# Optimization experiments

Measured on AMD Instinct MI355X. Metric: run time of the kernel, lower is better.

## Reference

```python
import jax, jax.numpy as jnp
import numpy as np

DIM = 1024
HID = 4 * DIM
N_EXPERTS = 8
TOP_K = 2


def setup_inputs() -> dict:
    key = jax.random.key(0)
    ks = jax.random.split(key, 8)
    s = lambda fan_in: 1.0 / np.sqrt(fan_in)
    x = jax.random.normal(ks[0], (2, 2048, DIM), dtype=jnp.float32)
    Wr = jax.random.uniform(ks[1], (DIM, N_EXPERTS), jnp.float32, -s(DIM), s(DIM))
    br = jnp.zeros((N_EXPERTS,), jnp.float32)
    W1 = jax.random.uniform(ks[2], (N_EXPERTS, DIM, HID), jnp.float32, -s(DIM), s(DIM))
    b1 = jnp.zeros((N_EXPERTS, HID), jnp.float32)
    W2 = jax.random.uniform(ks[3], (N_EXPERTS, HID, DIM), jnp.float32, -s(HID), s(HID))
    b2 = jnp.zeros((N_EXPERTS, DIM), jnp.float32)
    return {"x": x, "Wr": Wr, "br": br, "W1": W1, "b1": b1, "W2": W2, "b2": b2}


def reference(x, Wr, br, W1, b1, W2, b2):
    B, S, D = x.shape
    xf = x.reshape(-1, D)                      # [T, D]
    T = xf.shape[0]
    logits = xf @ Wr + br                      # [T, E]
    topw, sel = jax.lax.top_k(logits, TOP_K)   # [T, k]
    topw = jax.nn.softmax(topw, axis=-1)       # softmax over selected experts only
    # dense per-token, per-expert weight (0 for unselected experts)
    w_full = jnp.zeros((T, N_EXPERTS), xf.dtype).at[jnp.arange(T)[:, None], sel].add(topw)
    # run every expert densely (reference baseline), weighted combine
    h = jax.nn.gelu(jnp.einsum('td,edh->teh', xf, W1) + b1, approximate=False)  # [T,E,H]
    y = jnp.einsum('teh,ehd->ted', h, W2) + b2                                   # [T,E,D]
    out = jnp.einsum('ted,te->td', y, w_full)
    return out.reshape(B, S, D)
```

## Files before the change

### kernel.cpp

```cpp
#include <hip/hip_runtime.h>
#include <math.h>

#define DIM 1024
#define HID 4096
#define NE 8
#define NTOK 4096

typedef short s16x8 __attribute__((ext_vector_type(8)));
typedef float f32x4 __attribute__((ext_vector_type(4)));

__device__ __forceinline__ unsigned short f2bf(float f) {
  unsigned int u = __float_as_uint(f);
  u = u + 0x7fffu + ((u >> 16) & 1u);
  return (unsigned short)(u >> 16);
}

__device__ __forceinline__ void gll16(const void* g, void* l) {
  __builtin_amdgcn_global_load_lds(
      (const __attribute__((address_space(1))) unsigned int*)g,
      (__attribute__((address_space(3))) unsigned int*)l, 16, 0, 0);
}

__global__ __launch_bounds__(256) void zero_k(float4* out4, int* ctrl) {
  int i = blockIdx.x * 256 + threadIdx.x;
  out4[i] = make_float4(0.f, 0.f, 0.f, 0.f);
  if (i < 32) ctrl[i] = 0;
}

__global__ __launch_bounds__(256) void router_k(const float* __restrict__ x,
    const float* __restrict__ Wr, const float* __restrict__ br,
    short* __restrict__ xbf, int* __restrict__ ctrl,
    int* __restrict__ sel, float* __restrict__ selw) {
  __shared__ float lred[4 * NE];
  int t = blockIdx.x, tid = threadIdx.x;
  const float* xr = x + (size_t)t * DIM;
  float p[NE];
#pragma unroll
  for (int e = 0; e < NE; ++e) p[e] = 0.f;
#pragma unroll
  for (int it = 0; it < DIM / 256; ++it) {
    int d = it * 256 + tid;
    float xv = xr[d];
    xbf[(size_t)t * DIM + d] = (short)f2bf(xv);
#pragma unroll
    for (int e = 0; e < NE; ++e) p[e] += xv * Wr[d * NE + e];
  }
#pragma unroll
  for (int e = 0; e < NE; ++e) {
    float v = p[e];
#pragma unroll
    for (int off = 32; off > 0; off >>= 1) v += __shfl_down(v, off);
    if ((tid & 63) == 0) lred[(tid >> 6) * NE + e] = v;
  }
  __syncthreads();
  if (tid == 0) {
    float lg[NE];
#pragma unroll
    for (int e = 0; e < NE; ++e)
      lg[e] = lred[e] + lred[NE + e] + lred[2 * NE + e] + lred[3 * NE + e] + br[e];
    int b0 = 0; float v0 = lg[0];
    for (int e = 1; e < NE; ++e) if (lg[e] > v0) { v0 = lg[e]; b0 = e; }
    int b1i = -1; float v1 = -3.4e38f;
    for (int e = 0; e < NE; ++e) if (e != b0 && lg[e] > v1) { v1 = lg[e]; b1i = e; }
    float e1 = expf(v1 - v0);
    float inv = 1.f / (1.f + e1);
    sel[t * 2] = b0; sel[t * 2 + 1] = b1i;
    selw[t * 2] = inv; selw[t * 2 + 1] = e1 * inv;
    atomicAdd(&ctrl[b0], 1); atomicAdd(&ctrl[b1i], 1);
  }
}

__global__ void scan_k(int* ctrl) {
  if (threadIdx.x == 0) {
    int o = 0;
#pragma unroll
    for (int e = 0; e < NE; ++e) { ctrl[8 + e] = o; o += ctrl[e]; }
    ctrl[16] = o;
  }
}

__global__ __launch_bounds__(256) void build_k(const int* __restrict__ sel,
    const float* __restrict__ selw, int* ctrl,
    int* __restrict__ slot_tok, float* __restrict__ slot_w) {
  int t = blockIdx.x * 256 + threadIdx.x;
  if (t >= NTOK) return;
#pragma unroll
  for (int k = 0; k < 2; ++k) {
    int e = sel[t * 2 + k];
    int pos = atomicAdd(&ctrl[20 + e], 1);
    int s = ctrl[8 + e] + pos;
    slot_tok[s] = t;
    slot_w[s] = selw[t * 2 + k];
  }
}

__global__ __launch_bounds__(256) void tcvt_k(const float* __restrict__ src,
    short* __restrict__ dst, int K, int N) {
  __shared__ __attribute__((aligned(16))) short t[64][72];
  int e = blockIdx.z;
  int n0 = blockIdx.x * 64, k0 = blockIdx.y * 64;
  const float* s = src + (size_t)e * K * N;
  short* d = dst + (size_t)e * N * K;
  int tid = threadIdx.x;
#pragma unroll
  for (int i = 0; i < 4; ++i) {
    int c = tid + i * 256;
    int row = c >> 4, c4 = c & 15;
    float4 v = *(const float4*)&s[(size_t)(k0 + row) * N + n0 + c4 * 4];
    t[c4 * 4 + 0][row] = (short)f2bf(v.x);
    t[c4 * 4 + 1][row] = (short)f2bf(v.y);
    t[c4 * 4 + 2][row] = (short)f2bf(v.z);
    t[c4 * 4 + 3][row] = (short)f2bf(v.w);
  }
  __syncthreads();
#pragma unroll
  for (int i = 0; i < 2; ++i) {
    int c = tid + i * 256;
    int n = c >> 3, k8 = c & 7;
    *(s16x8*)&d[(size_t)(n0 + n) * K + k0 + k8 * 8] = *(const s16x8*)&t[n][k8 * 8];
  }
}

__global__ __launch_bounds__(256) void gemm1n_k(const short* __restrict__ xbf,
    const short* __restrict__ w1t, const float* __restrict__ b1,
    const int* __restrict__ ctrl, const int* __restrict__ slot_tok,
    short* __restrict__ h) {
  int e = blockIdx.z, my = blockIdx.y, bx = blockIdx.x;
  int cnt = ctrl[e];
  if (my * 128 >= cnt) return;
  int slot0 = ctrl[8 + e];
  int tid = threadIdx.x, lane = tid & 63;
  int wv = tid >> 6, wm = wv >> 1, wn = wv & 1;
  __shared__ __attribute__((aligned(16))) short ldsA[2][128 * 32];
  __shared__ __attribute__((aligned(16))) short ldsB[2][128 * 32];

  const short* ga[2]; const short* gb[2]; int lo[2];
#pragma unroll
  for (int i = 0; i < 2; ++i) {
    int c = tid + i * 256;
    int row = c >> 2;
    int cs = (c & 3) ^ (row & 3);
    int srow = min(my * 128 + row, cnt - 1);
    ga[i] = xbf + (size_t)slot_tok[slot0 + srow] * DIM + cs * 8;
    gb[i] = w1t + ((size_t)e * HID + bx * 128 + row) * DIM + cs * 8;
    lo[i] = c * 8;
  }
  int koff = ((lane >> 4) ^ (lane & 3)) * 8;

  f32x4 acc[4][4];
#pragma unroll
  for (int i = 0; i < 4; ++i)
#pragma unroll
    for (int j = 0; j < 4; ++j) acc[i][j] = (f32x4){0.f, 0.f, 0.f, 0.f};

#pragma unroll
  for (int i = 0; i < 2; ++i) { gll16(ga[i], &ldsA[0][lo[i]]); gll16(gb[i], &ldsB[0][lo[i]]); }
  __syncthreads();

  const int NT = DIM / 32;
  for (int t = 0; t < NT; ++t) {
    int buf = t & 1;
    if (t + 1 < NT) {
      int nb = buf ^ 1;
#pragma unroll
      for (int i = 0; i < 2; ++i) {
        gll16(ga[i] + (t + 1) * 32, &ldsA[nb][lo[i]]);
        gll16(gb[i] + (t + 1) * 32, &ldsB[nb][lo[i]]);
      }
    }
    s16x8 aF[4], bF[4];
#pragma unroll
    for (int i = 0; i < 4; ++i)
      aF[i] = *(const s16x8*)&ldsA[buf][(wm * 64 + i * 16 + (lane & 15)) * 32 + koff];
#pragma unroll
    for (int j = 0; j < 4; ++j)
      bF[j] = *(const s16x8*)&ldsB[buf][(wn * 64 + j * 16 + (lane & 15)) * 32 + koff];
#pragma unroll
    for (int i = 0; i < 4; ++i)
#pragma unroll
      for (int j = 0; j < 4; ++j)
        acc[i][j] = __builtin_amdgcn_mfma_f32_16x16x32_bf16(aF[i], bF[j], acc[i][j], 0, 0, 0);
    __syncthreads();
  }
#pragma unroll
  for (int i = 0; i < 4; ++i) {
#pragma unroll
    for (int r = 0; r < 4; ++r) {
      int row_l = wm * 64 + i * 16 + (lane >> 4) * 4 + r;
      int grow = my * 128 + row_l;
      if (grow < cnt) {
#pragma unroll
        for (int j = 0; j < 4; ++j) {
          int col = bx * 128 + wn * 64 + j * 16 + (lane & 15);
          float z = acc[i][j][r] + b1[e * HID + col];
          float g = 0.5f * z * (1.f + erff(z * 0.70710678118f));
          h[(size_t)(slot0 + grow) * HID + col] = (short)f2bf(g);
        }
      }
    }
  }
}

__global__ __launch_bounds__(256) void gemm2n_k(const short* __restrict__ h,
    const short* __restrict__ w2t, const float* __restrict__ b2,
    const int* __restrict__ ctrl, const int* __restrict__ slot_tok,
    const float* __restrict__ slot_w, float* __restrict__ out) {
  int e = blockIdx.z, my = blockIdx.y;
  int nx = blockIdx.x & 7, kc = blockIdx.x >> 3;
  int cnt = ctrl[e];
  if (my * 128 >= cnt) return;
  int slot0 = ctrl[8 + e];
  int tid = threadIdx.x, lane = tid & 63;
  int wv = tid >> 6, wm = wv >> 1, wn = wv & 1;
  __shared__ __attribute__((aligned(16))) short ldsA[2][128 * 32];
  __shared__ __attribute__((aligned(16))) short ldsB[2][128 * 32];
  __shared__ int stok[128];
  __shared__ float swt[128];
  if (tid < 128) {
    int srow = min(my * 128 + tid, cnt - 1);
    stok[tid] = slot_tok[slot0 + srow];
    swt[tid] = slot_w[slot0 + srow];
  }
  int k0 = kc * (HID / 4);
  const short* ga[2]; const short* gb[2]; int lo[2];
#pragma unroll
  for (int i = 0; i < 2; ++i) {
    int c = tid + i * 256;
    int row = c >> 2;
    int cs = (c & 3) ^ (row & 3);
    int srow = min(my * 128 + row, cnt - 1);
    ga[i] = h + (size_t)(slot0 + srow) * HID + k0 + cs * 8;
    gb[i] = w2t + ((size_t)e * DIM + nx * 128 + row) * HID + k0 + cs * 8;
    lo[i] = c * 8;
  }
  int koff = ((lane >> 4) ^ (lane & 3)) * 8;

  f32x4 acc[4][4];
#pragma unroll
  for (int i = 0; i < 4; ++i)
#pragma unroll
    for (int j = 0; j < 4; ++j) acc[i][j] = (f32x4){0.f, 0.f, 0.f, 0.f};

#pragma unroll
  for (int i = 0; i < 2; ++i) { gll16(ga[i], &ldsA[0][lo[i]]); gll16(gb[i], &ldsB[0][lo[i]]); }
  __syncthreads();

  const int NT = (HID / 4) / 32;
  for (int t = 0; t < NT; ++t) {
    int buf = t & 1;
    if (t + 1 < NT) {
      int nb = buf ^ 1;
#pragma unroll
      for (int i = 0; i < 2; ++i) {
        gll16(ga[i] + (t + 1) * 32, &ldsA[nb][lo[i]]);
        gll16(gb[i] + (t + 1) * 32, &ldsB[nb][lo[i]]);
      }
    }
    s16x8 aF[4], bF[4];
#pragma unroll
    for (int i = 0; i < 4; ++i)
      aF[i] = *(const s16x8*)&ldsA[buf][(wm * 64 + i * 16 + (lane & 15)) * 32 + koff];
#pragma unroll
    for (int j = 0; j < 4; ++j)
      bF[j] = *(const s16x8*)&ldsB[buf][(wn * 64 + j * 16 + (lane & 15)) * 32 + koff];
#pragma unroll
    for (int i = 0; i < 4; ++i)
#pragma unroll
      for (int j = 0; j < 4; ++j)
        acc[i][j] = __builtin_amdgcn_mfma_f32_16x16x32_bf16(aF[i], bF[j], acc[i][j], 0, 0, 0);
    __syncthreads();
  }
#pragma unroll
  for (int i = 0; i < 4; ++i) {
#pragma unroll
    for (int r = 0; r < 4; ++r) {
      int row_l = wm * 64 + i * 16 + (lane >> 4) * 4 + r;
      int grow = my * 128 + row_l;
      if (grow < cnt) {
        int tok = stok[row_l];
        float wrow = swt[row_l];
#pragma unroll
        for (int j = 0; j < 4; ++j) {
          int col = nx * 128 + wn * 64 + j * 16 + (lane & 15);
          float y = acc[i][j][r];
          if (kc == 0) y += b2[e * DIM + col];
          unsafeAtomicAdd(&out[(size_t)tok * DIM + col], wrow * y);
        }
      }
    }
  }
}

__global__ __launch_bounds__(256) void gemm1_k(const short* __restrict__ xbf,
    const float* __restrict__ W1, const float* __restrict__ b1,
    const int* __restrict__ ctrl, const int* __restrict__ slot_tok,
    short* __restrict__ h) {
  int e = blockIdx.z, my = blockIdx.y, bx = blockIdx.x;
  int cnt = ctrl[e];
  if (my * 128 >= cnt) return;
  int slot0 = ctrl[8 + e];
  int tid = threadIdx.x, lane = tid & 63;
  int wv = tid >> 6, wm = wv >> 1, wn = wv & 1;
  __shared__ __attribute__((aligned(16))) short ldsA[128 * 32];
  __shared__ __attribute__((aligned(16))) short ldsB[128 * 40];
  const short* ap[2]; short* la[2];
#pragma unroll
  for (int i = 0; i < 2; ++i) {
    int c = tid + i * 256;
    int row = c >> 2;
    int srow = min(my * 128 + row, cnt - 1);
    int tok = slot_tok[slot0 + srow];
    ap[i] = xbf + (size_t)tok * DIM + (c & 3) * 8;
    la[i] = &ldsA[c * 8];
  }
  int n0 = (tid & 63) * 2;
  int kg = tid >> 6;
  const float* bp = W1 + ((size_t)e * DIM + kg * 8) * HID + bx * 128 + n0;
  short* lb0 = &ldsB[(n0) * 40 + kg * 8];
  short* lb1 = &ldsB[(n0 + 1) * 40 + kg * 8];
  f32x4 acc[4][4];
#pragma unroll
  for (int i = 0; i < 4; ++i)
#pragma unroll
    for (int j = 0; j < 4; ++j) acc[i][j] = (f32x4){0.f, 0.f, 0.f, 0.f};
#pragma unroll 2
  for (int kt = 0; kt < DIM / 32; ++kt) {
    float2 fv[8];
#pragma unroll
    for (int kk = 0; kk < 8; ++kk) fv[kk] = *(const float2*)&bp[(size_t)kk * HID];
    __syncthreads();
    gll16(ap[0], la[0]); gll16(ap[1], la[1]);
    s16x8 v0, v1;
#pragma unroll
    for (int kk = 0; kk < 8; ++kk) { v0[kk] = (short)f2bf(fv[kk].x); v1[kk] = (short)f2bf(fv[kk].y); }
    *(s16x8*)lb0 = v0; *(s16x8*)lb1 = v1;
    asm volatile("s_waitcnt vmcnt(0)" ::: "memory");
    __syncthreads();
    s16x8 aF[4], bF[4];
#pragma unroll
    for (int i = 0; i < 4; ++i)
      aF[i] = *(const s16x8*)&ldsA[(wm * 64 + i * 16 + (lane & 15)) * 32 + (lane >> 4) * 8];
#pragma unroll
    for (int j = 0; j < 4; ++j)
      bF[j] = *(const s16x8*)&ldsB[(wn * 64 + j * 16 + (lane & 15)) * 40 + (lane >> 4) * 8];
#pragma unroll
    for (int i = 0; i < 4; ++i)
#pragma unroll
      for (int j = 0; j < 4; ++j)
        acc[i][j] = __builtin_amdgcn_mfma_f32_16x16x32_bf16(aF[i], bF[j], acc[i][j], 0, 0, 0);
    ap[0] += 32; ap[1] += 32; bp += (size_t)32 * HID;
  }
#pragma unroll
  for (int i = 0; i < 4; ++i)
#pragma unroll
    for (int r = 0; r < 4; ++r) {
      int row_l = wm * 64 + i * 16 + (lane >> 4) * 4 + r;
      int grow = my * 128 + row_l;
      if (grow < cnt)
#pragma unroll
        for (int j = 0; j < 4; ++j) {
          int col = bx * 128 + wn * 64 + j * 16 + (lane & 15);
          float z = acc[i][j][r] + b1[e * HID + col];
          float g = 0.5f * z * (1.f + erff(z * 0.70710678118f));
          h[(size_t)(slot0 + grow) * HID + col] = (short)f2bf(g);
        }
    }
}

__global__ __launch_bounds__(256) void gemm2_k(const short* __restrict__ h,
    const float* __restrict__ W2, const float* __restrict__ b2,
    const int* __restrict__ ctrl, const int* __restrict__ slot_tok,
    const float* __restrict__ slot_w, float* __restrict__ out) {
  int e = blockIdx.z, my = blockIdx.y, bx = blockIdx.x;
  int cnt = ctrl[e];
  if (my * 128 >= cnt) return;
  int slot0 = ctrl[8 + e];
  int tid = threadIdx.x, lane = tid & 63;
  int wv = tid >> 6, wm = wv >> 1, wn = wv & 1;
  __shared__ __attribute__((aligned(16))) short ldsA[128 * 32];
  __shared__ __attribute__((aligned(16))) short ldsB[128 * 40];
  __shared__ int stok[128];
  __shared__ float swt[128];
  if (tid < 128) {
    int srow = min(my * 128 + tid, cnt - 1);
    stok[tid] = slot_tok[slot0 + srow];
    swt[tid] = slot_w[slot0 + srow];
  }
  const short* ap[2]; short* la[2];
#pragma unroll
  for (int i = 0; i < 2; ++i) {
    int c = tid + i * 256;
    int row = c >> 2;
    int srow = min(my * 128 + row, cnt - 1);
    ap[i] = h + (size_t)(slot0 + srow) * HID + (c & 3) * 8;
    la[i] = &ldsA[c * 8];
  }
  int n0 = (tid & 63) * 2;
  int kg = tid >> 6;
  const float* bp = W2 + ((size_t)e * HID + kg * 8) * DIM + bx * 128 + n0;
  short* lb0 = &ldsB[(n0) * 40 + kg * 8];
  short* lb1 = &ldsB[(n0 + 1) * 40 + kg * 8];
  f32x4 acc[4][4];
#pragma unroll
  for (int i = 0; i < 4; ++i)
#pragma unroll
    for (int j = 0; j < 4; ++j) acc[i][j] = (f32x4){0.f, 0.f, 0.f, 0.f};
#pragma unroll 2
  for (int kt = 0; kt < HID / 32; ++kt) {
    float2 fv[8];
#pragma unroll
    for (int kk = 0; kk < 8; ++kk) fv[kk] = *(const float2*)&bp[(size_t)kk * DIM];
    __syncthreads();
    gll16(ap[0], la[0]); gll16(ap[1], la[1]);
    s16x8 v0, v1;
#pragma unroll
    for (int kk = 0; kk < 8; ++kk) { v0[kk] = (short)f2bf(fv[kk].x); v1[kk] = (short)f2bf(fv[kk].y); }
    *(s16x8*)lb0 = v0; *(s16x8*)lb1 = v1;
    asm volatile("s_waitcnt vmcnt(0)" ::: "memory");
    __syncthreads();
    s16x8 aF[4], bF[4];
#pragma unroll
    for (int i = 0; i < 4; ++i)
      aF[i] = *(const s16x8*)&ldsA[(wm * 64 + i * 16 + (lane & 15)) * 32 + (lane >> 4) * 8];
#pragma unroll
    for (int j = 0; j < 4; ++j)
      bF[j] = *(const s16x8*)&ldsB[(wn * 64 + j * 16 + (lane & 15)) * 40 + (lane >> 4) * 8];
#pragma unroll
    for (int i = 0; i < 4; ++i)
#pragma unroll
      for (int j = 0; j < 4; ++j)
        acc[i][j] = __builtin_amdgcn_mfma_f32_16x16x32_bf16(aF[i], bF[j], acc[i][j], 0, 0, 0);
    ap[0] += 32; ap[1] += 32; bp += (size_t)32 * DIM;
  }
#pragma unroll
  for (int i = 0; i < 4; ++i)
#pragma unroll
    for (int r = 0; r < 4; ++r) {
      int row_l = wm * 64 + i * 16 + (lane >> 4) * 4 + r;
      int grow = my * 128 + row_l;
      if (grow < cnt) {
        int tok = stok[row_l];
        float wrow = swt[row_l];
#pragma unroll
        for (int j = 0; j < 4; ++j) {
          int col = bx * 128 + wn * 64 + j * 16 + (lane & 15);
          float y = acc[i][j][r] + b2[e * DIM + col];
          unsafeAtomicAdd(&out[(size_t)tok * DIM + col], wrow * y);
        }
      }
    }
}

extern "C" void kernel_launch(void* const* d_in, const int* in_sizes, int n_in,
                              void* d_out, int out_size, void* d_ws, size_t ws_size,
                              hipStream_t stream) {
  const float* x  = (const float*)d_in[0];
  const float* Wr = (const float*)d_in[1];
  const float* br = (const float*)d_in[2];
  const float* W1 = (const float*)d_in[3];
  const float* b1 = (const float*)d_in[4];
  const float* W2 = (const float*)d_in[5];
  const float* b2 = (const float*)d_in[6];
  float* out = (float*)d_out;

  char* ws = (char*)d_ws;
  const size_t MiB = 1024 * 1024;
  int*   ctrl     = (int*)(ws);
  int*   sel      = (int*)(ws + 1024);
  float* selw     = (float*)(ws + 33792);
  int*   slot_tok = (int*)(ws + 66560);
  float* slot_w   = (float*)(ws + 99328);
  short* xbf      = (short*)(ws + 1 * MiB);
  short* h        = (short*)(ws + 16 * MiB);
  short* w1t      = (short*)(ws + 80 * MiB);
  short* w2t      = (short*)(ws + 144 * MiB);
  bool fat = ws_size >= 208 * MiB;

  zero_k<<<(NTOK * DIM / 4) / 256, 256, 0, stream>>>((float4*)out, ctrl);
  router_k<<<NTOK, 256, 0, stream>>>(x, Wr, br, xbf, ctrl, sel, selw);
  scan_k<<<1, 64, 0, stream>>>(ctrl);
  build_k<<<NTOK / 256, 256, 0, stream>>>(sel, selw, ctrl, slot_tok, slot_w);
  if (fat) {
    tcvt_k<<<dim3(HID / 64, DIM / 64, NE), 256, 0, stream>>>(W1, w1t, DIM, HID);
    tcvt_k<<<dim3(DIM / 64, HID / 64, NE), 256, 0, stream>>>(W2, w2t, HID, DIM);
    gemm1n_k<<<dim3(HID / 128, NTOK / 128, NE), 256, 0, stream>>>(xbf, w1t, b1, ctrl, slot_tok, h);
    gemm2n_k<<<dim3((DIM / 128) * 4, NTOK / 128, NE), 256, 0, stream>>>(h, w2t, b2, ctrl, slot_tok, slot_w, out);
  } else {
    gemm1_k<<<dim3(HID / 128, NTOK / 128, NE), 256, 0, stream>>>(xbf, W1, b1, ctrl, slot_tok, h);
    gemm2_k<<<dim3(DIM / 128, NTOK / 128, NE), 256, 0, stream>>>(h, W2, b2, ctrl, slot_tok, slot_w, out);
  }
}
```

Measured before the change: 841.3 us.

## Register-staged prefetch pipeline, XCD-aware block swizzle, and halve gemm2 split-K

Replaces the global_load_lds double-buffering in both expert GEMMs with a register-staged pipeline. Global loads for tile t+2 are issued into registers, then written to LDS after the MFMAs of tile t, separated by one explicit barrier per step. It also flattens the launch grid and applies a swizzle so that consecutive blocks on the same XCD share an expert and N-tile, aiming for better L2 reuse of weights. gemm2 switches from 4-way to 2-way split-K, which halves the atomic adds to the output at the cost of fewer blocks. The register staging uses more VGPRs and relies on the grid dimensions matching the swizzle arithmetic exactly.

```diff
diff --git a/kernel.cpp b/kernel.cpp
--- a/kernel.cpp
+++ b/kernel.cpp
@@ -121,11 +121,63 @@
   }
 }
 
+#define BAR_CLUSTER                                                            \
+  asm volatile("s_waitcnt lgkmcnt(0)" ::: "memory");                           \
+  __builtin_amdgcn_s_barrier();                                                \
+  asm volatile("" ::: "memory");                                               \
+  __builtin_amdgcn_sched_barrier(0);
+
+#define GBODY(T, NTV, BUFR, BUFW, RS0, RS1, RS2, RS3, RW0, RW1, RW2, RW3)      \
+  {                                                                            \
+    if ((T) + 2 < (NTV)) {                                                     \
+      int off_ = ((T) + 2) * 32;                                               \
+      RS0 = *(const s16x8*)(ga[0] + off_);                                     \
+      RS1 = *(const s16x8*)(ga[1] + off_);                                     \
+      RS2 = *(const s16x8*)(gb[0] + off_);                                     \
+      RS3 = *(const s16x8*)(gb[1] + off_);                                     \
+    }                                                                          \
+    s16x8 aF[4], bF[4];                                                        \
+    _Pragma("unroll") for (int i_ = 0; i_ < 4; ++i_)                           \
+      aF[i_] = *(const s16x8*)&ldsA[BUFR][(wm * 64 + i_ * 16 + (lane & 15)) * 32 + koff]; \
+    _Pragma("unroll") for (int j_ = 0; j_ < 4; ++j_)                           \
+      bF[j_] = *(const s16x8*)&ldsB[BUFR][(wn * 64 + j_ * 16 + (lane & 15)) * 32 + koff]; \
+    _Pragma("unroll") for (int i_ = 0; i_ < 4; ++i_)                           \
+      _Pragma("unroll") for (int j_ = 0; j_ < 4; ++j_)                         \
+        acc[i_][j_] = __builtin_amdgcn_mfma_f32_16x16x32_bf16(aF[i_], bF[j_], acc[i_][j_], 0, 0, 0); \
+    if ((T) + 1 < (NTV)) {                                                     \
+      *(s16x8*)&ldsA[BUFW][lo[0]] = RW0;                                       \
+      *(s16x8*)&ldsA[BUFW][lo[1]] = RW1;                                       \
+      *(s16x8*)&ldsB[BUFW][lo[0]] = RW2;                                       \
+      *(s16x8*)&ldsB[BUFW][lo[1]] = RW3;                                       \
+    }                                                                          \
+    BAR_CLUSTER                                                                \
+  }
+
+#define GPROLOGUE                                                              \
+  s16x8 rA0, rA1, rA2, rA3, rB0, rB1, rB2, rB3;                                \
+  rA0 = *(const s16x8*)(ga[0]);                                                \
+  rA1 = *(const s16x8*)(ga[1]);                                                \
+  rA2 = *(const s16x8*)(gb[0]);                                                \
+  rA3 = *(const s16x8*)(gb[1]);                                                \
+  rB0 = *(const s16x8*)(ga[0] + 32);                                           \
+  rB1 = *(const s16x8*)(ga[1] + 32);                                           \
+  rB2 = *(const s16x8*)(gb[0] + 32);                                           \
+  rB3 = *(const s16x8*)(gb[1] + 32);                                           \
+  *(s16x8*)&ldsA[0][lo[0]] = rA0;                                              \
+  *(s16x8*)&ldsA[0][lo[1]] = rA1;                                              \
+  *(s16x8*)&ldsB[0][lo[0]] = rA2;                                              \
+  *(s16x8*)&ldsB[0][lo[1]] = rA3;                                              \
+  BAR_CLUSTER
+
 __global__ __launch_bounds__(256) void gemm1n_k(const short* __restrict__ xbf,
     const short* __restrict__ w1t, const float* __restrict__ b1,
     const int* __restrict__ ctrl, const int* __restrict__ slot_tok,
     short* __restrict__ h) {
-  int e = blockIdx.z, my = blockIdx.y, bx = blockIdx.x;
+  int bid = blockIdx.x;
+  int swz = (bid & 7) * 1024 + (bid >> 3);
+  int nx = swz >> 8;
+  int e = (swz >> 5) & 7;
+  int my = swz & 31;
   int cnt = ctrl[e];
   if (my * 128 >= cnt) return;
   int slot0 = ctrl[8 + e];
@@ -142,7 +194,7 @@
     int cs = (c & 3) ^ (row & 3);
     int srow = min(my * 128 + row, cnt - 1);
     ga[i] = xbf + (size_t)slot_tok[slot0 + srow] * DIM + cs * 8;
-    gb[i] = w1t + ((size_t)e * HID + bx * 128 + row) * DIM + cs * 8;
+    gb[i] = w1t + ((size_t)e * HID + nx * 128 + row) * DIM + cs * 8;
     lo[i] = c * 8;
   }
   int koff = ((lane >> 4) ^ (lane & 3)) * 8;
@@ -153,35 +205,13 @@
 #pragma unroll
     for (int j = 0; j < 4; ++j) acc[i][j] = (f32x4){0.f, 0.f, 0.f, 0.f};
 
-#pragma unroll
-  for (int i = 0; i < 2; ++i) { gll16(ga[i], &ldsA[0][lo[i]]); gll16(gb[i], &ldsB[0][lo[i]]); }
-  __syncthreads();
-
+  GPROLOGUE
   const int NT = DIM / 32;
-  for (int t = 0; t < NT; ++t) {
-    int buf = t & 1;
-    if (t + 1 < NT) {
-      int nb = buf ^ 1;
-#pragma unroll
-      for (int i = 0; i < 2; ++i) {
-        gll16(ga[i] + (t + 1) * 32, &ldsA[nb][lo[i]]);
-        gll16(gb[i] + (t + 1) * 32, &ldsB[nb][lo[i]]);
-      }
-    }
-    s16x8 aF[4], bF[4];
-#pragma unroll
-    for (int i = 0; i < 4; ++i)
-      aF[i] = *(const s16x8*)&ldsA[buf][(wm * 64 + i * 16 + (lane & 15)) * 32 + koff];
-#pragma unroll
-    for (int j = 0; j < 4; ++j)
-      bF[j] = *(const s16x8*)&ldsB[buf][(wn * 64 + j * 16 + (lane & 15)) * 32 + koff];
-#pragma unroll
-    for (int i = 0; i < 4; ++i)
-#pragma unroll
-      for (int j = 0; j < 4; ++j)
-        acc[i][j] = __builtin_amdgcn_mfma_f32_16x16x32_bf16(aF[i], bF[j], acc[i][j], 0, 0, 0);
-    __syncthreads();
-  }
+  for (int t = 0; t < NT; t += 2) {
+    GBODY(t,     NT, 0, 1, rA0, rA1, rA2, rA3, rB0, rB1, rB2, rB3)
+    GBODY(t + 1, NT, 1, 0, rB0, rB1, rB2, rB3, rA0, rA1, rA2, rA3)
+  }
+
 #pragma unroll
   for (int i = 0; i < 4; ++i) {
 #pragma unroll
@@ -191,7 +221,7 @@
       if (grow < cnt) {
 #pragma unroll
         for (int j = 0; j < 4; ++j) {
-          int col = bx * 128 + wn * 64 + j * 16 + (lane & 15);
+          int col = nx * 128 + wn * 64 + j * 16 + (lane & 15);
           float z = acc[i][j][r] + b1[e * HID + col];
           float g = 0.5f * z * (1.f + erff(z * 0.70710678118f));
           h[(size_t)(slot0 + grow) * HID + col] = (short)f2bf(g);
@@ -205,8 +235,12 @@
     const short* __restrict__ w2t, const float* __restrict__ b2,
     const int* __restrict__ ctrl, const int* __restrict__ slot_tok,
     const float* __restrict__ slot_w, float* __restrict__ out) {
-  int e = blockIdx.z, my = blockIdx.y;
-  int nx = blockIdx.x & 7, kc = blockIdx.x >> 3;
+  int bid = blockIdx.x;
+  int swz = (bid & 7) * 512 + (bid >> 3);
+  int kc = swz >> 11;
+  int nx = (swz >> 8) & 7;
+  int e = (swz >> 5) & 7;
+  int my = swz & 31;
   int cnt = ctrl[e];
   if (my * 128 >= cnt) return;
   int slot0 = ctrl[8 + e];
@@ -221,7 +255,7 @@
     stok[tid] = slot_tok[slot0 + srow];
     swt[tid] = slot_w[slot0 + srow];
   }
-  int k0 = kc * (HID / 4);
+  int k0 = kc * (HID / 2);
   const short* ga[2]; const short* gb[2]; int lo[2];
 #pragma unroll
   for (int i = 0; i < 2; ++i) {
@@ -241,35 +275,13 @@
 #pragma unroll
     for (int j = 0; j < 4; ++j) acc[i][j] = (f32x4){0.f, 0.f, 0.f, 0.f};
 
-#pragma unroll
-  for (int i = 0; i < 2; ++i) { gll16(ga[i], &ldsA[0][lo[i]]); gll16(gb[i], &ldsB[0][lo[i]]); }
-  __syncthreads();
-
-  const int NT = (HID / 4) / 32;
-  for (int t = 0; t < NT; ++t) {
-    int buf = t & 1;
-    if (t + 1 < NT) {
-      int nb = buf ^ 1;
-#pragma unroll
-      for (int i = 0; i < 2; ++i) {
-        gll16(ga[i] + (t + 1) * 32, &ldsA[nb][lo[i]]);
-        gll16(gb[i] + (t + 1) * 32, &ldsB[nb][lo[i]]);
-      }
-    }
-    s16x8 aF[4], bF[4];
-#pragma unroll
-    for (int i = 0; i < 4; ++i)
-      aF[i] = *(const s16x8*)&ldsA[buf][(wm * 64 + i * 16 + (lane & 15)) * 32 + koff];
-#pragma unroll
-    for (int j = 0; j < 4; ++j)
-      bF[j] = *(const s16x8*)&ldsB[buf][(wn * 64 + j * 16 + (lane & 15)) * 32 + koff];
-#pragma unroll
-    for (int i = 0; i < 4; ++i)
-#pragma unroll
-      for (int j = 0; j < 4; ++j)
-        acc[i][j] = __builtin_amdgcn_mfma_f32_16x16x32_bf16(aF[i], bF[j], acc[i][j], 0, 0, 0);
-    __syncthreads();
-  }
+  GPROLOGUE
+  const int NT = (HID / 2) / 32;
+  for (int t = 0; t < NT; t += 2) {
+    GBODY(t,     NT, 0, 1, rA0, rA1, rA2, rA3, rB0, rB1, rB2, rB3)
+    GBODY(t + 1, NT, 1, 0, rB0, rB1, rB2, rB3, rA0, rA1, rA2, rA3)
+  }
+
 #pragma unroll
   for (int i = 0; i < 4; ++i) {
 #pragma unroll
@@ -483,8 +495,8 @@
   if (fat) {
     tcvt_k<<<dim3(HID / 64, DIM / 64, NE), 256, 0, stream>>>(W1, w1t, DIM, HID);
     tcvt_k<<<dim3(DIM / 64, HID / 64, NE), 256, 0, stream>>>(W2, w2t, HID, DIM);
-    gemm1n_k<<<dim3(HID / 128, NTOK / 128, NE), 256, 0, stream>>>(xbf, w1t, b1, ctrl, slot_tok, h);
-    gemm2n_k<<<dim3((DIM / 128) * 4, NTOK / 128, NE), 256, 0, stream>>>(h, w2t, b2, ctrl, slot_tok, slot_w, out);
+    gemm1n_k<<<32 * 32 * NE, 256, 0, stream>>>(xbf, w1t, b1, ctrl, slot_tok, h);
+    gemm2n_k<<<8 * 32 * NE * 2, 256, 0, stream>>>(h, w2t, b2, ctrl, slot_tok, slot_w, out);
   } else {
     gemm1_k<<<dim3(HID / 128, NTOK / 128, NE), 256, 0, stream>>>(xbf, W1, b1, ctrl, slot_tok, h);
     gemm2_k<<<dim3(DIM / 128, NTOK / 128, NE), 256, 0, stream>>>(h, W2, b2, ctrl, slot_tok, slot_w, out);
```

New measurement: 840.5 us. About the same (-0.1%).
